# Performance work log

Measured on AMD Instinct MI355X. Metric: run time of the kernel, lower is better.

Reference implementation:

```python
import jax, jax.numpy as jnp
import numpy as np

N_NODES = 100000  # 2 node types x 50k
N_EDGES = 1600000


def setup_inputs() -> dict:
    key = jax.random.key(0)
    ks = jax.random.split(key, 16)
    feat0 = jax.random.normal(ks[0], (50000, 128), dtype=jnp.float32)
    feat1 = jax.random.normal(ks[1], (50000, 256), dtype=jnp.float32)
    edge_rows = jax.random.randint(ks[2], (N_EDGES,), 0, N_NODES, dtype=jnp.int32)
    edge_cols = jax.random.randint(ks[3], (N_EDGES,), 0, N_NODES, dtype=jnp.int32)
    edge_w = jax.random.uniform(ks[4], (N_EDGES,), dtype=jnp.float32)
    # fc_list: Linear(feat_dim, in_feat=128) per node type (torch Linear: x @ W.T + b)
    fc0_w = jax.random.normal(ks[5], (128, 128), dtype=jnp.float32) * 0.1
    fc0_b = jnp.zeros((128,), dtype=jnp.float32)
    fc1_w = jax.random.normal(ks[6], (128, 256), dtype=jnp.float32) * 0.07
    fc1_b = jnp.zeros((128,), dtype=jnp.float32)
    # GCNConv weights: W is [in, out] used as features @ W
    W1 = jax.random.normal(ks[7], (128, 128), dtype=jnp.float32) * 0.1  # in_feat -> 2*out_feat
    b1 = jnp.zeros((128,), dtype=jnp.float32)
    W2 = jax.random.normal(ks[8], (128, 64), dtype=jnp.float32) * 0.1   # 2*out_feat -> out_feat
    b2 = jnp.zeros((64,), dtype=jnp.float32)
    # predict: Linear(out_feat=64, num_class=8)
    pred_w = jax.random.normal(ks[9], (8, 64), dtype=jnp.float32) * 0.1
    pred_b = jnp.zeros((8,), dtype=jnp.float32)
    return {
        "feat0": feat0, "feat1": feat1,
        "fc0_w": fc0_w, "fc0_b": fc0_b, "fc1_w": fc1_w, "fc1_b": fc1_b,
        "W1": W1, "b1": b1, "W2": W2, "b2": b2,
        "pred_w": pred_w, "pred_b": pred_b,
        "edge_rows": edge_rows, "edge_cols": edge_cols, "edge_w": edge_w,
    }


def _spmm(edge_rows, edge_cols, edge_w, dense):
    # (sparse adj) @ dense : gather source rows, scale, scatter-add to dest rows
    msgs = dense[edge_cols] * edge_w[:, None]  # [E, F]
    return jax.ops.segment_sum(msgs, edge_rows, num_segments=N_NODES)


def reference(feat0, feat1, fc0_w, fc0_b, fc1_w, fc1_b, W1, b1, W2, b2,
              pred_w, pred_b, edge_rows, edge_cols, edge_w):
    # per-type projection (dropout is identity at p=0.0 / eval), then concat over nodes
    x0 = feat0 @ fc0_w.T + fc0_b
    x1 = feat1 @ fc1_w.T + fc1_b
    x = jnp.concatenate([x0, x1], axis=0)  # [N, 128]
    # GCN layer 1: relu(spmm(adj, x @ W1) + b1)
    x = jax.nn.relu(_spmm(edge_rows, edge_cols, edge_w, x @ W1) + b1)
    # GCN layer 2
    x = jax.nn.relu(_spmm(edge_rows, edge_cols, edge_w, x @ W2) + b2)
    # predict head
    return x @ pred_w.T + pred_b  # [N, num_class]
```

## Files before the change

kernel.cpp:

```cpp
#include <hip/hip_runtime.h>
#include <hip/hip_bf16.h>

#define N_NODES 100000
#define N_TYPE  50000
#define NB1     192
#define EPB1    8334
#define NBUCK2  196
#define CAP2    9216

typedef short bf16x8 __attribute__((ext_vector_type(8)));
typedef float f32x4  __attribute__((ext_vector_type(4)));
typedef unsigned short u16x4 __attribute__((ext_vector_type(4)));

__device__ inline unsigned short f2bf(float f) {
  union { float f; unsigned u; } x; x.f = f;
  unsigned r = (x.u + 0x7fff + ((x.u >> 16) & 1)) >> 16;
  return (unsigned short)r;
}
__device__ inline float bf2f(unsigned short h) {
  union { unsigned u; float f; } x; x.u = ((unsigned)h) << 16;
  return x.f;
}

__global__ __launch_bounds__(256) void prep_small_kernel(
    const float* __restrict__ fc0_w, const float* __restrict__ fc1_w,
    const float* __restrict__ fc0_b, const float* __restrict__ fc1_b,
    const float* __restrict__ W1, const float* __restrict__ W2,
    const float* __restrict__ pred_w,
    unsigned short* __restrict__ M0T, unsigned short* __restrict__ M1T,
    unsigned short* __restrict__ W2T, unsigned short* __restrict__ pwT,
    float* __restrict__ cb) {
  int idx = blockIdx.x * 256 + threadIdx.x;
  if (idx < 16384) {
    int i = idx >> 7, j = idx & 127;
    float s = 0.f;
    #pragma unroll 4
    for (int o = 0; o < 128; ++o) s = fmaf(fc0_w[o * 128 + i], W1[o * 128 + j], s);
    M0T[j * 128 + i] = f2bf(s);
  } else if (idx < 49152) {
    int r = idx - 16384;
    int i = r >> 7, j = r & 127;
    float s = 0.f;
    #pragma unroll 4
    for (int o = 0; o < 128; ++o) s = fmaf(fc1_w[o * 256 + i], W1[o * 128 + j], s);
    M1T[j * 256 + i] = f2bf(s);
  } else if (idx < 57344) {
    int r = idx - 49152;
    int k = r >> 6, n = r & 63;
    W2T[n * 128 + k] = f2bf(W2[k * 64 + n]);
  } else if (idx < 57600) {
    int r = idx - 57344;
    int t = r >> 7, j = r & 127;
    const float* bb = t ? fc1_b : fc0_b;
    float s = 0.f;
    for (int o = 0; o < 128; ++o) s = fmaf(bb[o], W1[o * 128 + j], s);
    cb[r] = s;
  } else if (idx < 58624) {
    int r = idx - 57600;
    int n = r >> 6, k = r & 63;
    pwT[r] = (n < 8) ? f2bf(pred_w[n * 64 + k]) : (unsigned short)0;
  }
}

template <int NC, int KTOT>
__global__ __launch_bounds__(256) void mfma_gemm_kernel(
    const float* __restrict__ A, const unsigned short* __restrict__ BT,
    const float* __restrict__ bc, unsigned short* __restrict__ Cout, int M) {
  constexpr int NREP = NC / 32;
  __shared__ unsigned short As[64 * 128];
  __shared__ unsigned short Bs[NC * 128];

  const int tid = threadIdx.x;
  const int row0 = blockIdx.x * 64;
  const int wave = tid >> 6, lane = tid & 63;
  const int wr = wave >> 1, wc = wave & 1;
  const int lm = lane & 15;
  const int lk16 = (lane >> 4) * 16;

  f32x4 acc[2][NREP];
  #pragma unroll
  for (int i = 0; i < 2; ++i)
    #pragma unroll
    for (int j = 0; j < NREP; ++j) acc[i][j] = (f32x4){0.f, 0.f, 0.f, 0.f};

  for (int kc = 0; kc < KTOT; kc += 128) {
    if (kc) __syncthreads();
    {
      const int r = tid >> 2;
      const int cg = tid & 3;
      int gr = row0 + r; if (gr > M - 1) gr = M - 1;
      const float* arow = A + (size_t)gr * KTOT + kc;
      char* asrow = (char*)As + r * 256;
      const int swz = (r & 7) << 4;
      #pragma unroll
      for (int i = 0; i < 8; ++i) {
        const int c = i * 4 + cg;
        float4 v = *(const float4*)(arow + c * 4);
        u16x4 q = {f2bf(v.x), f2bf(v.y), f2bf(v.z), f2bf(v.w)};
        *(u16x4*)(asrow + ((c * 8) ^ swz)) = q;
      }
    }
    {
      constexpr int CHUNKS = NC * 16;
      #pragma unroll
      for (int i = 0; i < CHUNKS / 256; ++i) {
        const int id = i * 256 + tid;
        const int n = id >> 4, k16 = id & 15;
        const uint4 w = *(const uint4*)((const char*)BT + ((size_t)n * KTOT + kc) * 2 + k16 * 16);
        *(uint4*)((char*)Bs + ((n * 256 + k16 * 16) ^ ((n & 7) << 4))) = w;
      }
    }
    __syncthreads();
    #pragma unroll
    for (int ks = 0; ks < 4; ++ks) {
      bf16x8 a[2];
      #pragma unroll
      for (int m = 0; m < 2; ++m) {
        const int r = wr * 32 + m * 16 + lm;
        a[m] = *(bf16x8*)((char*)As + ((r * 256 + ks * 64 + lk16) ^ ((r & 7) << 4)));
      }
      #pragma unroll
      for (int j = 0; j < NREP; ++j) {
        const int n = wc * (NC / 2) + j * 16 + lm;
        const bf16x8 b = *(bf16x8*)((char*)Bs + ((n * 256 + ks * 64 + lk16) ^ ((n & 7) << 4)));
        acc[0][j] = __builtin_amdgcn_mfma_f32_16x16x32_bf16(a[0], b, acc[0][j], 0, 0, 0);
        acc[1][j] = __builtin_amdgcn_mfma_f32_16x16x32_bf16(a[1], b, acc[1][j], 0, 0, 0);
      }
    }
  }
  #pragma unroll
  for (int m = 0; m < 2; ++m) {
    const int gr0 = row0 + wr * 32 + m * 16 + (lane >> 4) * 4;
    #pragma unroll
    for (int j = 0; j < NREP; ++j) {
      const int col = wc * (NC / 2) + j * 16 + lm;
      const float cbv = bc[col];
      #pragma unroll
      for (int i = 0; i < 4; ++i) {
        const int gr = gr0 + i;
        if (gr < M) Cout[(size_t)gr * NC + col] = f2bf(acc[m][j][i] + cbv);
      }
    }
  }
}

__global__ __launch_bounds__(256) void gemmA64_kernel(
    const unsigned short* __restrict__ A, const unsigned short* __restrict__ BT,
    unsigned short* __restrict__ Cout, int M) {
  __shared__ unsigned short As[64 * 128];
  __shared__ unsigned short Bs[64 * 128];
  const int tid = threadIdx.x;
  const int row0 = blockIdx.x * 64;
  const int wave = tid >> 6, lane = tid & 63;
  const int wr = wave >> 1, wc = wave & 1;
  const int lm = lane & 15, lk16 = (lane >> 4) * 16;
  {
    const int r = tid >> 2, cg = tid & 3;
    int gr = row0 + r; if (gr > M - 1) gr = M - 1;
    const uint4* arow = (const uint4*)(A + (size_t)gr * 128);
    const int swz = (r & 7) << 4;
    #pragma unroll
    for (int i = 0; i < 4; ++i) {
      const int c16 = i * 4 + cg;
      const uint4 w = arow[c16];
      *(uint4*)((char*)As + ((r * 256 + c16 * 16) ^ swz)) = w;
    }
  }
  #pragma unroll
  for (int i = 0; i < 4; ++i) {
    const int id = i * 256 + tid;
    const int n = id >> 4, k16 = id & 15;
    const uint4 w = *(const uint4*)((const char*)BT + n * 256 + k16 * 16);
    *(uint4*)((char*)Bs + ((n * 256 + k16 * 16) ^ ((n & 7) << 4))) = w;
  }
  __syncthreads();
  f32x4 acc[2][2];
  #pragma unroll
  for (int i = 0; i < 2; ++i)
    #pragma unroll
    for (int j = 0; j < 2; ++j) acc[i][j] = (f32x4){0.f, 0.f, 0.f, 0.f};
  #pragma unroll
  for (int ks = 0; ks < 4; ++ks) {
    bf16x8 a[2];
    #pragma unroll
    for (int m = 0; m < 2; ++m) {
      const int r = wr * 32 + m * 16 + lm;
      a[m] = *(bf16x8*)((char*)As + ((r * 256 + ks * 64 + lk16) ^ ((r & 7) << 4)));
    }
    #pragma unroll
    for (int j = 0; j < 2; ++j) {
      const int n = wc * 32 + j * 16 + lm;
      const bf16x8 b = *(bf16x8*)((char*)Bs + ((n * 256 + ks * 64 + lk16) ^ ((n & 7) << 4)));
      acc[0][j] = __builtin_amdgcn_mfma_f32_16x16x32_bf16(a[0], b, acc[0][j], 0, 0, 0);
      acc[1][j] = __builtin_amdgcn_mfma_f32_16x16x32_bf16(a[1], b, acc[1][j], 0, 0, 0);
    }
  }
  #pragma unroll
  for (int m = 0; m < 2; ++m) {
    const int gr0 = row0 + wr * 32 + m * 16 + (lane >> 4) * 4;
    #pragma unroll
    for (int j = 0; j < 2; ++j) {
      const int col = wc * 32 + j * 16 + lm;
      #pragma unroll
      for (int i = 0; i < 4; ++i) {
        const int gr = gr0 + i;
        if (gr < M) Cout[(size_t)gr * 64 + col] = f2bf(acc[m][j][i]);
      }
    }
  }
}

__global__ __launch_bounds__(512) void hist1_kernel(
    const int* __restrict__ erow, int* __restrict__ gh, int nE) {
  __shared__ int lh[256];
  const int t = threadIdx.x;
  const int e0 = blockIdx.x * EPB1;
  const int e1 = min(e0 + EPB1, nE);
  for (int i = t; i < 256; i += 512) lh[i] = 0;
  __syncthreads();
  for (int i = e0 + t; i < e1; i += 512) atomicAdd(&lh[erow[i] >> 9], 1);
  __syncthreads();
  for (int i = t; i < NBUCK2; i += 512) gh[i * NB1 + blockIdx.x] = lh[i];
}

__global__ __launch_bounds__(256) void scan_kernel(
    const int* __restrict__ gh, int* __restrict__ gbase, int* __restrict__ bcnt) {
  const int t = threadIdx.x;
  if (t >= NBUCK2) return;
  int run = t * CAP2;
  for (int blk = 0; blk < NB1; ++blk) {
    gbase[blk * 256 + t] = run;
    run += gh[t * NB1 + blk];
  }
  bcnt[t] = run - t * CAP2;
}

__global__ __launch_bounds__(512) void scatter1_kernel(
    const int* __restrict__ erow, const int* __restrict__ ecol,
    const float* __restrict__ ew, const int* __restrict__ gbase,
    uint2* __restrict__ tmp, int nE) {
  __shared__ int lh[256];
  __shared__ int lbase[256];
  const int t = threadIdx.x;
  const int e0 = blockIdx.x * EPB1;
  const int e1 = min(e0 + EPB1, nE);
  for (int i = t; i < 256; i += 512) {
    lh[i] = 0;
    lbase[i] = (i < NBUCK2) ? gbase[blockIdx.x * 256 + i] : 0;
  }
  __syncthreads();
  for (int i = e0 + t; i < e1; i += 512) {
    const int r = erow[i];
    const int b = r >> 9;
    const int pos = lbase[b] + atomicAdd(&lh[b], 1);
    const unsigned short bw = f2bf(ew[i]);
    const unsigned rec = ((unsigned)ecol[i] << 15) | (unsigned)bw;
    tmp[pos] = make_uint2(rec, (unsigned)r);
  }
}

__global__ __launch_bounds__(512) void part2_kernel(
    const int* __restrict__ bcnt, const uint2* __restrict__ tmp,
    unsigned* __restrict__ spack, int2* __restrict__ row_se, int N) {
  __shared__ int hist[512];
  __shared__ int scn[512];
  __shared__ int cur[512];
  const int b = blockIdx.x;
  const int r0 = b << 9;
  const int t = threadIdx.x;
  const int base = b * CAP2;
  const int cnt = bcnt[b];
  const uint2* rec = tmp + base;
  hist[t] = 0;
  __syncthreads();
  for (int i = t; i < cnt; i += 512)
    atomicAdd(&hist[(int)rec[i].y - r0], 1);
  __syncthreads();
  const int v = hist[t];
  scn[t] = v;
  __syncthreads();
  #pragma unroll
  for (int off = 1; off < 512; off <<= 1) {
    int y = (t >= off) ? scn[t - off] : 0;
    __syncthreads();
    scn[t] += y;
    __syncthreads();
  }
  const int excl = base + scn[t] - v;
  const int r = r0 + t;
  if (r < N) row_se[r] = make_int2(excl, excl + v);
  cur[t] = excl;
  __syncthreads();
  for (int i = t; i < cnt; i += 512) {
    const uint2 rc = rec[i];
    const int pos = atomicAdd(&cur[(int)rc.y - r0], 1);
    spack[pos] = rc.x;
  }
}

__global__ __launch_bounds__(256) void spmm1_kernel(
    const unsigned short* __restrict__ h, const int2* __restrict__ row_se,
    const unsigned* __restrict__ spack, const float* __restrict__ b1,
    unsigned short* __restrict__ g1, int M) {
  const int r = (blockIdx.x * 256 + threadIdx.x) >> 5;
  const int lane = threadIdx.x & 31;
  if (r >= M) return;
  const int2 se = row_se[r];
  f32x4 acc = (f32x4){0.f, 0.f, 0.f, 0.f};
  int j = se.x;
  for (; j + 3 < se.y; j += 4) {
    const unsigned rc0 = spack[j], rc1 = spack[j + 1];
    const unsigned rc2 = spack[j + 2], rc3 = spack[j + 3];
    const u16x4 v0 = *(const u16x4*)(h + (size_t)(rc0 >> 15) * 128 + lane * 4);
    const u16x4 v1 = *(const u16x4*)(h + (size_t)(rc1 >> 15) * 128 + lane * 4);
    const u16x4 v2 = *(const u16x4*)(h + (size_t)(rc2 >> 15) * 128 + lane * 4);
    const u16x4 v3 = *(const u16x4*)(h + (size_t)(rc3 >> 15) * 128 + lane * 4);
    const float w0 = bf2f((unsigned short)(rc0 & 0x7fff));
    const float w1 = bf2f((unsigned short)(rc1 & 0x7fff));
    const float w2 = bf2f((unsigned short)(rc2 & 0x7fff));
    const float w3 = bf2f((unsigned short)(rc3 & 0x7fff));
    #pragma unroll
    for (int k = 0; k < 4; ++k) {
      acc[k] = fmaf(bf2f(v0[k]), w0, acc[k]);
      acc[k] = fmaf(bf2f(v1[k]), w1, acc[k]);
      acc[k] = fmaf(bf2f(v2[k]), w2, acc[k]);
      acc[k] = fmaf(bf2f(v3[k]), w3, acc[k]);
    }
  }
  for (; j < se.y; ++j) {
    const unsigned rc0 = spack[j];
    const u16x4 v0 = *(const u16x4*)(h + (size_t)(rc0 >> 15) * 128 + lane * 4);
    const float w0 = bf2f((unsigned short)(rc0 & 0x7fff));
    #pragma unroll
    for (int k = 0; k < 4; ++k) acc[k] = fmaf(bf2f(v0[k]), w0, acc[k]);
  }
  const float4 bb = *(const float4*)(b1 + lane * 4);
  u16x4 o;
  o[0] = f2bf(fmaxf(acc[0] + bb.x, 0.f));
  o[1] = f2bf(fmaxf(acc[1] + bb.y, 0.f));
  o[2] = f2bf(fmaxf(acc[2] + bb.z, 0.f));
  o[3] = f2bf(fmaxf(acc[3] + bb.w, 0.f));
  *(u16x4*)(g1 + (size_t)r * 128 + lane * 4) = o;
}

__global__ __launch_bounds__(256) void spmm2_kernel(
    const unsigned short* __restrict__ h2, const int2* __restrict__ row_se,
    const unsigned* __restrict__ spack, const float* __restrict__ b2,
    unsigned short* __restrict__ g2, int M) {
  const int r = (blockIdx.x * 256 + threadIdx.x) >> 5;
  const int lane = threadIdx.x & 31;
  if (r >= M) return;
  const int2 se = row_se[r];
  float2 acc = make_float2(0.f, 0.f);
  int j = se.x;
  for (; j + 3 < se.y; j += 4) {
    const unsigned rc0 = spack[j], rc1 = spack[j + 1];
    const unsigned rc2 = spack[j + 2], rc3 = spack[j + 3];
    const ushort2 v0 = *(const ushort2*)(h2 + (size_t)(rc0 >> 15) * 64 + lane * 2);
    const ushort2 v1 = *(const ushort2*)(h2 + (size_t)(rc1 >> 15) * 64 + lane * 2);
    const ushort2 v2 = *(const ushort2*)(h2 + (size_t)(rc2 >> 15) * 64 + lane * 2);
    const ushort2 v3 = *(const ushort2*)(h2 + (size_t)(rc3 >> 15) * 64 + lane * 2);
    const float w0 = bf2f((unsigned short)(rc0 & 0x7fff));
    const float w1 = bf2f((unsigned short)(rc1 & 0x7fff));
    const float w2 = bf2f((unsigned short)(rc2 & 0x7fff));
    const float w3 = bf2f((unsigned short)(rc3 & 0x7fff));
    acc.x = fmaf(bf2f(v0.x), w0, acc.x);
    acc.y = fmaf(bf2f(v0.y), w0, acc.y);
    acc.x = fmaf(bf2f(v1.x), w1, acc.x);
    acc.y = fmaf(bf2f(v1.y), w1, acc.y);
    acc.x = fmaf(bf2f(v2.x), w2, acc.x);
    acc.y = fmaf(bf2f(v2.y), w2, acc.y);
    acc.x = fmaf(bf2f(v3.x), w3, acc.x);
    acc.y = fmaf(bf2f(v3.y), w3, acc.y);
  }
  for (; j < se.y; ++j) {
    const unsigned rc0 = spack[j];
    const ushort2 v0 = *(const ushort2*)(h2 + (size_t)(rc0 >> 15) * 64 + lane * 2);
    const float w0 = bf2f((unsigned short)(rc0 & 0x7fff));
    acc.x = fmaf(bf2f(v0.x), w0, acc.x);
    acc.y = fmaf(bf2f(v0.y), w0, acc.y);
  }
  const float a0 = fmaxf(acc.x + b2[lane * 2], 0.f);
  const float a1 = fmaxf(acc.y + b2[lane * 2 + 1], 0.f);
  ushort2 o;
  o.x = f2bf(a0);
  o.y = f2bf(a1);
  *(ushort2*)(g2 + (size_t)r * 64 + lane * 2) = o;
}

__global__ __launch_bounds__(256) void head_kernel(
    const unsigned short* __restrict__ g2, const unsigned short* __restrict__ pwT,
    const float* __restrict__ pred_b, float* __restrict__ out, int M) {
  __shared__ unsigned short As[64 * 64];
  __shared__ unsigned short Bs[16 * 64];
  const int tid = threadIdx.x;
  const int wave = tid >> 6, lane = tid & 63;
  const int row0 = blockIdx.x * 64;
  if (tid < 128) {
    const int n = tid >> 3, k16 = tid & 7;
    const uint4 w = *(const uint4*)((const char*)pwT + n * 128 + k16 * 16);
    *(uint4*)((char*)Bs + ((n * 128 + k16 * 16) ^ ((n & 7) << 4))) = w;
  }
  #pragma unroll
  for (int i = 0; i < 2; ++i) {
    const int id = i * 256 + tid;
    const int rr = id >> 3, k16 = id & 7;
    int gr = row0 + rr; if (gr > M - 1) gr = M - 1;
    const uint4 w = *(const uint4*)(g2 + (size_t)gr * 64 + k16 * 8);
    *(uint4*)((char*)As + ((rr * 128 + k16 * 16) ^ ((rr & 7) << 4))) = w;
  }
  __syncthreads();
  const int lm = lane & 15, lk16 = (lane >> 4) * 16;
  f32x4 acc4 = (f32x4){0.f, 0.f, 0.f, 0.f};
  #pragma unroll
  for (int ks = 0; ks < 2; ++ks) {
    const int rrow = wave * 16 + lm;
    const bf16x8 a = *(bf16x8*)((char*)As + ((rrow * 128 + ks * 64 + lk16) ^ ((rrow & 7) << 4)));
    const bf16x8 b = *(bf16x8*)((char*)Bs + ((lm * 128 + ks * 64 + lk16) ^ ((lm & 7) << 4)));
    acc4 = __builtin_amdgcn_mfma_f32_16x16x32_bf16(a, b, acc4, 0, 0, 0);
  }
  if (lm < 8) {
    const float pbv = pred_b[lm];
    const int gr0 = row0 + wave * 16 + (lane >> 4) * 4;
    #pragma unroll
    for (int i = 0; i < 4; ++i) {
      const int gr = gr0 + i;
      if (gr < M) out[(size_t)gr * 8 + lm] = acc4[i] + pbv;
    }
  }
}

extern "C" void kernel_launch(void* const* d_in, const int* in_sizes, int n_in,
                              void* d_out, int out_size, void* d_ws, size_t ws_size,
                              hipStream_t stream) {
  const float* feat0  = (const float*)d_in[0];
  const float* feat1  = (const float*)d_in[1];
  const float* fc0_w  = (const float*)d_in[2];
  const float* fc0_b  = (const float*)d_in[3];
  const float* fc1_w  = (const float*)d_in[4];
  const float* fc1_b  = (const float*)d_in[5];
  const float* W1     = (const float*)d_in[6];
  const float* b1     = (const float*)d_in[7];
  const float* W2     = (const float*)d_in[8];
  const float* b2     = (const float*)d_in[9];
  const float* pred_w = (const float*)d_in[10];
  const float* pred_b = (const float*)d_in[11];
  const int*   erow   = (const int*)d_in[12];
  const int*   ecol   = (const int*)d_in[13];
  const float* ew     = (const float*)d_in[14];
  float* out = (float*)d_out;
  const int nE = in_sizes[12];
  const int N = N_NODES;

  char* ws = (char*)d_ws;
  size_t off = 0;
  unsigned short* M0T = (unsigned short*)(ws + off); off += 32768;
  unsigned short* M1T = (unsigned short*)(ws + off); off += 65536;
  unsigned short* W2T = (unsigned short*)(ws + off); off += 16384;
  unsigned short* pwT = (unsigned short*)(ws + off); off += 2048;
  float* cb   = (float*)(ws + off); off += 1024;
  int* gh     = (int*)(ws + off); off += (size_t)NBUCK2 * NB1 * 4;
  int* gbase  = (int*)(ws + off); off += (size_t)NB1 * 256 * 4;
  int* bcnt   = (int*)(ws + off); off += 1024;
  uint2* tmp  = (uint2*)(ws + off); off += (size_t)NBUCK2 * CAP2 * 8;
  unsigned* spack = (unsigned*)(ws + off); off += (size_t)NBUCK2 * CAP2 * 4;
  int2* row_se = (int2*)(ws + off); off += (size_t)N * 8;
  unsigned short* h  = (unsigned short*)(ws + off); off += (size_t)N * 128 * 2;
  unsigned short* g1 = (unsigned short*)(ws + off); off += (size_t)N * 128 * 2;
  unsigned short* h2 = (unsigned short*)(ws + off); off += (size_t)N * 64 * 2;
  unsigned short* g2 = (unsigned short*)(ws + off); off += (size_t)N * 64 * 2;

  hipLaunchKernelGGL(hist1_kernel, dim3(NB1), dim3(512), 0, stream, erow, gh, nE);
  hipLaunchKernelGGL(scan_kernel, dim3(1), dim3(256), 0, stream, gh, gbase, bcnt);
  hipLaunchKernelGGL(scatter1_kernel, dim3(NB1), dim3(512), 0, stream,
                     erow, ecol, ew, gbase, tmp, nE);
  hipLaunchKernelGGL(part2_kernel, dim3(NBUCK2), dim3(512), 0, stream,
                     bcnt, tmp, spack, row_se, N);

  hipLaunchKernelGGL(prep_small_kernel, dim3(229), dim3(256), 0, stream,
                     fc0_w, fc1_w, fc0_b, fc1_b, W1, W2, pred_w,
                     M0T, M1T, W2T, pwT, cb);
  hipLaunchKernelGGL((mfma_gemm_kernel<128, 128>), dim3((N_TYPE + 63) / 64), dim3(256),
                     0, stream, feat0, M0T, cb, h, N_TYPE);
  hipLaunchKernelGGL((mfma_gemm_kernel<128, 256>), dim3((N_TYPE + 63) / 64), dim3(256),
                     0, stream, feat1, M1T, cb + 128, h + (size_t)N_TYPE * 128, N_TYPE);
  hipLaunchKernelGGL(spmm1_kernel, dim3((N * 32 + 255) / 256), dim3(256), 0, stream,
                     h, row_se, spack, b1, g1, N);
  hipLaunchKernelGGL(gemmA64_kernel, dim3((N + 63) / 64), dim3(256), 0, stream,
                     g1, W2T, h2, N);
  hipLaunchKernelGGL(spmm2_kernel, dim3((N * 32 + 255) / 256), dim3(256), 0, stream,
                     h2, row_se, spack, b2, g2, N);
  hipLaunchKernelGGL(head_kernel, dim3((N + 63) / 64), dim3(256), 0, stream,
                     g2, pwT, pred_b, out, N);
}
```

Measured before the change: 209.5 us.

## Slice feature tables by 16 columns and pin slices to XCDs in SpMM

Feature matrices h, g1, h2 and g2 are stored column-sliced ([slice][node][16]), so each 16-column slice is contiguous. The SpMM kernels now assign blocks so that bid&7 selects the slice, which places each slice's gather table on one XCD and shrinks the per-XCD L2 working set for the random gathers. The producer GEMMs and the head kernel are changed to write and read the sliced layout. The trade-off is that the edge list is now read once per slice (8x for layer 1, 4x for layer 2) and each gather moves only 32 bytes, with nontemporal loads on spack.

```diff
diff --git a/kernel.cpp b/kernel.cpp
--- a/kernel.cpp
+++ b/kernel.cpp
@@ -65,7 +65,8 @@
 template <int NC, int KTOT>
 __global__ __launch_bounds__(256) void mfma_gemm_kernel(
     const float* __restrict__ A, const unsigned short* __restrict__ BT,
-    const float* __restrict__ bc, unsigned short* __restrict__ Cout, int M) {
+    const float* __restrict__ bc, unsigned short* __restrict__ Cout,
+    int row_off, int M) {
   constexpr int NREP = NC / 32;
   __shared__ unsigned short As[64 * 128];
   __shared__ unsigned short Bs[NC * 128];
@@ -138,7 +139,9 @@
       #pragma unroll
       for (int i = 0; i < 4; ++i) {
         const int gr = gr0 + i;
-        if (gr < M) Cout[(size_t)gr * NC + col] = f2bf(acc[m][j][i] + cbv);
+        if (gr < M)
+          Cout[((size_t)(col >> 4) * N_NODES + row_off + gr) * 16 + (col & 15)] =
+              f2bf(acc[m][j][i] + cbv);
       }
     }
   }
@@ -157,13 +160,15 @@
   {
     const int r = tid >> 2, cg = tid & 3;
     int gr = row0 + r; if (gr > M - 1) gr = M - 1;
-    const uint4* arow = (const uint4*)(A + (size_t)gr * 128);
     const int swz = (r & 7) << 4;
     #pragma unroll
-    for (int i = 0; i < 4; ++i) {
-      const int c16 = i * 4 + cg;
-      const uint4 w = arow[c16];
-      *(uint4*)((char*)As + ((r * 256 + c16 * 16) ^ swz)) = w;
+    for (int i = 0; i < 2; ++i) {
+      const int s = cg * 2 + i;
+      const unsigned short* src = A + ((size_t)s * N_NODES + gr) * 16;
+      const uint4 w0 = *(const uint4*)(src);
+      const uint4 w1 = *(const uint4*)(src + 8);
+      *(uint4*)((char*)As + ((r * 256 + s * 32) ^ swz)) = w0;
+      *(uint4*)((char*)As + ((r * 256 + s * 32 + 16) ^ swz)) = w1;
     }
   }
   #pragma unroll
@@ -204,7 +209,8 @@
       #pragma unroll
       for (int i = 0; i < 4; ++i) {
         const int gr = gr0 + i;
-        if (gr < M) Cout[(size_t)gr * 64 + col] = f2bf(acc[m][j][i]);
+        if (gr < M)
+          Cout[((size_t)(col >> 4) * N_NODES + gr) * 16 + (col & 15)] = f2bf(acc[m][j][i]);
       }
     }
   }
@@ -299,97 +305,85 @@
 }
 
 __global__ __launch_bounds__(256) void spmm1_kernel(
-    const unsigned short* __restrict__ h, const int2* __restrict__ row_se,
+    const unsigned short* __restrict__ h_sl, const int2* __restrict__ row_se,
     const unsigned* __restrict__ spack, const float* __restrict__ b1,
-    unsigned short* __restrict__ g1, int M) {
-  const int r = (blockIdx.x * 256 + threadIdx.x) >> 5;
-  const int lane = threadIdx.x & 31;
+    unsigned short* __restrict__ g1_sl, int M) {
+  const int bid = blockIdx.x;
+  const int s = bid & 7;
+  const int row0 = (bid >> 3) * 16;
+  const int tid = threadIdx.x;
+  const int grp = tid >> 4, lane = tid & 15;
+  const int r = row0 + grp;
   if (r >= M) return;
   const int2 se = row_se[r];
-  f32x4 acc = (f32x4){0.f, 0.f, 0.f, 0.f};
+  const unsigned short* tab = h_sl + (size_t)s * N_NODES * 16 + lane;
+  float acc = 0.f;
   int j = se.x;
   for (; j + 3 < se.y; j += 4) {
-    const unsigned rc0 = spack[j], rc1 = spack[j + 1];
-    const unsigned rc2 = spack[j + 2], rc3 = spack[j + 3];
-    const u16x4 v0 = *(const u16x4*)(h + (size_t)(rc0 >> 15) * 128 + lane * 4);
-    const u16x4 v1 = *(const u16x4*)(h + (size_t)(rc1 >> 15) * 128 + lane * 4);
-    const u16x4 v2 = *(const u16x4*)(h + (size_t)(rc2 >> 15) * 128 + lane * 4);
-    const u16x4 v3 = *(const u16x4*)(h + (size_t)(rc3 >> 15) * 128 + lane * 4);
-    const float w0 = bf2f((unsigned short)(rc0 & 0x7fff));
-    const float w1 = bf2f((unsigned short)(rc1 & 0x7fff));
-    const float w2 = bf2f((unsigned short)(rc2 & 0x7fff));
-    const float w3 = bf2f((unsigned short)(rc3 & 0x7fff));
-    #pragma unroll
-    for (int k = 0; k < 4; ++k) {
-      acc[k] = fmaf(bf2f(v0[k]), w0, acc[k]);
-      acc[k] = fmaf(bf2f(v1[k]), w1, acc[k]);
-      acc[k] = fmaf(bf2f(v2[k]), w2, acc[k]);
-      acc[k] = fmaf(bf2f(v3[k]), w3, acc[k]);
-    }
+    const unsigned rc0 = __builtin_nontemporal_load(spack + j);
+    const unsigned rc1 = __builtin_nontemporal_load(spack + j + 1);
+    const unsigned rc2 = __builtin_nontemporal_load(spack + j + 2);
+    const unsigned rc3 = __builtin_nontemporal_load(spack + j + 3);
+    const unsigned short v0 = tab[(size_t)(rc0 >> 15) * 16];
+    const unsigned short v1 = tab[(size_t)(rc1 >> 15) * 16];
+    const unsigned short v2 = tab[(size_t)(rc2 >> 15) * 16];
+    const unsigned short v3 = tab[(size_t)(rc3 >> 15) * 16];
+    acc = fmaf(bf2f(v0), bf2f((unsigned short)(rc0 & 0x7fff)), acc);
+    acc = fmaf(bf2f(v1), bf2f((unsigned short)(rc1 & 0x7fff)), acc);
+    acc = fmaf(bf2f(v2), bf2f((unsigned short)(rc2 & 0x7fff)), acc);
+    acc = fmaf(bf2f(v3), bf2f((unsigned short)(rc3 & 0x7fff)), acc);
   }
   for (; j < se.y; ++j) {
-    const unsigned rc0 = spack[j];
-    const u16x4 v0 = *(const u16x4*)(h + (size_t)(rc0 >> 15) * 128 + lane * 4);
-    const float w0 = bf2f((unsigned short)(rc0 & 0x7fff));
-    #pragma unroll
-    for (int k = 0; k < 4; ++k) acc[k] = fmaf(bf2f(v0[k]), w0, acc[k]);
-  }
-  const float4 bb = *(const float4*)(b1 + lane * 4);
-  u16x4 o;
-  o[0] = f2bf(fmaxf(acc[0] + bb.x, 0.f));
-  o[1] = f2bf(fmaxf(acc[1] + bb.y, 0.f));
-  o[2] = f2bf(fmaxf(acc[2] + bb.z, 0.f));
-  o[3] = f2bf(fmaxf(acc[3] + bb.w, 0.f));
-  *(u16x4*)(g1 + (size_t)r * 128 + lane * 4) = o;
+    const unsigned rc0 = __builtin_nontemporal_load(spack + j);
+    const unsigned short v0 = tab[(size_t)(rc0 >> 15) * 16];
+    acc = fmaf(bf2f(v0), bf2f((unsigned short)(rc0 & 0x7fff)), acc);
+  }
+  const float a = fmaxf(acc + b1[s * 16 + lane], 0.f);
+  __builtin_nontemporal_store(f2bf(a), g1_sl + ((size_t)s * N_NODES + r) * 16 + lane);
 }
 
 __global__ __launch_bounds__(256) void spmm2_kernel(
-    const unsigned short* __restrict__ h2, const int2* __restrict__ row_se,
+    const unsigned short* __restrict__ h2_sl, const int2* __restrict__ row_se,
     const unsigned* __restrict__ spack, const float* __restrict__ b2,
-    unsigned short* __restrict__ g2, int M) {
-  const int r = (blockIdx.x * 256 + threadIdx.x) >> 5;
-  const int lane = threadIdx.x & 31;
+    unsigned short* __restrict__ g2_sl, int M) {
+  const int bid = blockIdx.x;
+  const int xcd = bid & 7;
+  const int s = xcd >> 1;
+  const int half = xcd & 1;
+  const int row0 = ((bid >> 3) * 2 + half) * 16;
+  const int tid = threadIdx.x;
+  const int grp = tid >> 4, lane = tid & 15;
+  const int r = row0 + grp;
   if (r >= M) return;
   const int2 se = row_se[r];
-  float2 acc = make_float2(0.f, 0.f);
+  const unsigned short* tab = h2_sl + (size_t)s * N_NODES * 16 + lane;
+  float acc = 0.f;
   int j = se.x;
   for (; j + 3 < se.y; j += 4) {
-    const unsigned rc0 = spack[j], rc1 = spack[j + 1];
-    const unsigned rc2 = spack[j + 2], rc3 = spack[j + 3];
-    const ushort2 v0 = *(const ushort2*)(h2 + (size_t)(rc0 >> 15) * 64 + lane * 2);
-    const ushort2 v1 = *(const ushort2*)(h2 + (size_t)(rc1 >> 15) * 64 + lane * 2);
-    const ushort2 v2 = *(const ushort2*)(h2 + (size_t)(rc2 >> 15) * 64 + lane * 2);
-    const ushort2 v3 = *(const ushort2*)(h2 + (size_t)(rc3 >> 15) * 64 + lane * 2);
-    const float w0 = bf2f((unsigned short)(rc0 & 0x7fff));
-    const float w1 = bf2f((unsigned short)(rc1 & 0x7fff));
-    const float w2 = bf2f((unsigned short)(rc2 & 0x7fff));
-    const float w3 = bf2f((unsigned short)(rc3 & 0x7fff));
-    acc.x = fmaf(bf2f(v0.x), w0, acc.x);
-    acc.y = fmaf(bf2f(v0.y), w0, acc.y);
-    acc.x = fmaf(bf2f(v1.x), w1, acc.x);
-    acc.y = fmaf(bf2f(v1.y), w1, acc.y);
-    acc.x = fmaf(bf2f(v2.x), w2, acc.x);
-    acc.y = fmaf(bf2f(v2.y), w2, acc.y);
-    acc.x = fmaf(bf2f(v3.x), w3, acc.x);
-    acc.y = fmaf(bf2f(v3.y), w3, acc.y);
+    const unsigned rc0 = __builtin_nontemporal_load(spack + j);
+    const unsigned rc1 = __builtin_nontemporal_load(spack + j + 1);
+    const unsigned rc2 = __builtin_nontemporal_load(spack + j + 2);
+    const unsigned rc3 = __builtin_nontemporal_load(spack + j + 3);
+    const unsigned short v0 = tab[(size_t)(rc0 >> 15) * 16];
+    const unsigned short v1 = tab[(size_t)(rc1 >> 15) * 16];
+    const unsigned short v2 = tab[(size_t)(rc2 >> 15) * 16];
+    const unsigned short v3 = tab[(size_t)(rc3 >> 15) * 16];
+    acc = fmaf(bf2f(v0), bf2f((unsigned short)(rc0 & 0x7fff)), acc);
+    acc = fmaf(bf2f(v1), bf2f((unsigned short)(rc1 & 0x7fff)), acc);
+    acc = fmaf(bf2f(v2), bf2f((unsigned short)(rc2 & 0x7fff)), acc);
+    acc = fmaf(bf2f(v3), bf2f((unsigned short)(rc3 & 0x7fff)), acc);
   }
   for (; j < se.y; ++j) {
-    const unsigned rc0 = spack[j];
-    const ushort2 v0 = *(const ushort2*)(h2 + (size_t)(rc0 >> 15) * 64 + lane * 2);
-    const float w0 = bf2f((unsigned short)(rc0 & 0x7fff));
-    acc.x = fmaf(bf2f(v0.x), w0, acc.x);
-    acc.y = fmaf(bf2f(v0.y), w0, acc.y);
-  }
-  const float a0 = fmaxf(acc.x + b2[lane * 2], 0.f);
-  const float a1 = fmaxf(acc.y + b2[lane * 2 + 1], 0.f);
-  ushort2 o;
-  o.x = f2bf(a0);
-  o.y = f2bf(a1);
-  *(ushort2*)(g2 + (size_t)r * 64 + lane * 2) = o;
+    const unsigned rc0 = __builtin_nontemporal_load(spack + j);
+    const unsigned short v0 = tab[(size_t)(rc0 >> 15) * 16];
+    acc = fmaf(bf2f(v0), bf2f((unsigned short)(rc0 & 0x7fff)), acc);
+  }
+  const float a = fmaxf(acc + b2[s * 16 + lane], 0.f);
+  __builtin_nontemporal_store(f2bf(a), g2_sl + ((size_t)s * N_NODES + r) * 16 + lane);
 }
 
 __global__ __launch_bounds__(256) void head_kernel(
-    const unsigned short* __restrict__ g2, const unsigned short* __restrict__ pwT,
+    const unsigned short* __restrict__ g2_sl, const unsigned short* __restrict__ pwT,
     const float* __restrict__ pred_b, float* __restrict__ out, int M) {
   __shared__ unsigned short As[64 * 64];
   __shared__ unsigned short Bs[16 * 64];
@@ -406,7 +400,8 @@
     const int id = i * 256 + tid;
     const int rr = id >> 3, k16 = id & 7;
     int gr = row0 + rr; if (gr > M - 1) gr = M - 1;
-    const uint4 w = *(const uint4*)(g2 + (size_t)gr * 64 + k16 * 8);
+    const int s = k16 >> 1, jj = k16 & 1;
+    const uint4 w = *(const uint4*)(g2_sl + ((size_t)s * N_NODES + gr) * 16 + jj * 8);
     *(uint4*)((char*)As + ((rr * 128 + k16 * 16) ^ ((rr & 7) << 4))) = w;
   }
   __syncthreads();
@@ -465,10 +460,10 @@
   uint2* tmp  = (uint2*)(ws + off); off += (size_t)NBUCK2 * CAP2 * 8;
   unsigned* spack = (unsigned*)(ws + off); off += (size_t)NBUCK2 * CAP2 * 4;
   int2* row_se = (int2*)(ws + off); off += (size_t)N * 8;
-  unsigned short* h  = (unsigned short*)(ws + off); off += (size_t)N * 128 * 2;
-  unsigned short* g1 = (unsigned short*)(ws + off); off += (size_t)N * 128 * 2;
-  unsigned short* h2 = (unsigned short*)(ws + off); off += (size_t)N * 64 * 2;
-  unsigned short* g2 = (unsigned short*)(ws + off); off += (size_t)N * 64 * 2;
+  unsigned short* h_sl  = (unsigned short*)(ws + off); off += (size_t)N * 128 * 2;
+  unsigned short* g1_sl = (unsigned short*)(ws + off); off += (size_t)N * 128 * 2;
+  unsigned short* h2_sl = (unsigned short*)(ws + off); off += (size_t)N * 64 * 2;
+  unsigned short* g2_sl = (unsigned short*)(ws + off); off += (size_t)N * 64 * 2;
 
   hipLaunchKernelGGL(hist1_kernel, dim3(NB1), dim3(512), 0, stream, erow, gh, nE);
   hipLaunchKernelGGL(scan_kernel, dim3(1), dim3(256), 0, stream, gh, gbase, bcnt);
@@ -481,15 +476,15 @@
                      fc0_w, fc1_w, fc0_b, fc1_b, W1, W2, pred_w,
                      M0T, M1T, W2T, pwT, cb);
   hipLaunchKernelGGL((mfma_gemm_kernel<128, 128>), dim3((N_TYPE + 63) / 64), dim3(256),
-                     0, stream, feat0, M0T, cb, h, N_TYPE);
+                     0, stream, feat0, M0T, cb, h_sl, 0, N_TYPE);
   hipLaunchKernelGGL((mfma_gemm_kernel<128, 256>), dim3((N_TYPE + 63) / 64), dim3(256),
-                     0, stream, feat1, M1T, cb + 128, h + (size_t)N_TYPE * 128, N_TYPE);
-  hipLaunchKernelGGL(spmm1_kernel, dim3((N * 32 + 255) / 256), dim3(256), 0, stream,
-                     h, row_se, spack, b1, g1, N);
+                     0, stream, feat1, M1T, cb + 128, h_sl, N_TYPE, N_TYPE);
+  hipLaunchKernelGGL(spmm1_kernel, dim3(8 * ((N + 15) / 16)), dim3(256), 0, stream,
+                     h_sl, row_se, spack, b1, g1_sl, N);
   hipLaunchKernelGGL(gemmA64_kernel, dim3((N + 63) / 64), dim3(256), 0, stream,
-                     g1, W2T, h2, N);
-  hipLaunchKernelGGL(spmm2_kernel, dim3((N * 32 + 255) / 256), dim3(256), 0, stream,
-                     h2, row_se, spack, b2, g2, N);
+                     g1_sl, W2T, h2_sl, N);
+  hipLaunchKernelGGL(spmm2_kernel, dim3(8 * ((N + 31) / 32)), dim3(256), 0, stream,
+                     h2_sl, row_se, spack, b2, g2_sl, N);
   hipLaunchKernelGGL(head_kernel, dim3((N + 63) / 64), dim3(256), 0, stream,
-                     g2, pwT, pred_b, out, N);
-}
+                     g2_sl, pwT, pred_b, out, N);
+}
```

After: 399.6 us. +90.7%, slower.
